# Kernel optimization log

Hardware: AMD Instinct MI355X
Metric: run time of the kernel (lower is better)

Reference implementation:

```python
import jax, jax.numpy as jnp
import numpy as np

D_MODEL = 1024
NUM_HEADS = 16
DEPTH = D_MODEL // NUM_HEADS
B, S = 2, 2048


def setup_inputs() -> dict:
    key = jax.random.key(0)
    ks = jax.random.split(key, 12)
    s = 1.0 / np.sqrt(D_MODEL)
    return {
        "query": jax.random.normal(ks[0], (B, S, D_MODEL), jnp.float32),
        "key": jax.random.normal(ks[1], (B, S, D_MODEL), jnp.float32),
        "value": jax.random.normal(ks[2], (B, S, D_MODEL), jnp.float32),
        "mask": jax.random.randint(ks[3], (B, S), 0, 2, jnp.int32),
        "Wq": jax.random.normal(ks[4], (D_MODEL, D_MODEL), jnp.float32) * s,
        "bq": jnp.zeros((D_MODEL,), jnp.float32),
        "Wk": jax.random.normal(ks[5], (D_MODEL, D_MODEL), jnp.float32) * s,
        "bk": jnp.zeros((D_MODEL,), jnp.float32),
        "Wv": jax.random.normal(ks[6], (D_MODEL, D_MODEL), jnp.float32) * s,
        "bv": jnp.zeros((D_MODEL,), jnp.float32),
        "Wo": jax.random.normal(ks[7], (D_MODEL, D_MODEL), jnp.float32) * s,
        "bo": jnp.zeros((D_MODEL,), jnp.float32),
    }


def _split_heads(x):
    # [B, S, D] -> [B, H, S, depth]
    b, s, _ = x.shape
    return x.reshape(b, s, NUM_HEADS, DEPTH).transpose(0, 2, 1, 3)


def reference(query, key, value, mask, Wq, bq, Wk, bk, Wv, bv, Wo, bo):
    q = _split_heads(query @ Wq.T + bq)
    k = _split_heads(key @ Wk.T + bk)
    v = _split_heads(value @ Wv.T + bv)
    scale = 1.0 / jnp.sqrt(jnp.float32(DEPTH))
    # [B, H, Sq, Sk]
    logits = jnp.einsum("bhqd,bhkd->bhqk", q, k) * scale
    logits = logits + mask.astype(logits.dtype)[:, None, None, :] * (-1e9)
    attn = jax.nn.softmax(logits, axis=-1)
    out = jnp.einsum("bhqk,bhkd->bhqd", attn, v)
    out = out.transpose(0, 2, 1, 3).reshape(query.shape[0], -1, D_MODEL)
    return out @ Wo.T + bo
```

## Files before the change

kernel.cpp:

```cpp
#include <hip/hip_runtime.h>

typedef _Float16 half8 __attribute__((ext_vector_type(8)));
typedef _Float16 half4 __attribute__((ext_vector_type(4)));
typedef __fp16  fp16x2 __attribute__((ext_vector_type(2)));
typedef float floatx4 __attribute__((ext_vector_type(4)));

#define D_MODEL 1024
#define NHEAD   16
#define DH      64
#define BATCH   2
#define SEQ     2048
#define M_TOT   4096

#define SCALE_L2E 0.18033688011112042f
#define MASK_L2E  (-1.4426950408889634e9f)

#define GLD_LDS16(g, l)                                                          \
  __builtin_amdgcn_global_load_lds(                                              \
      (const __attribute__((address_space(1))) void*)(g),                        \
      (__attribute__((address_space(3))) void*)(l), 16, 0, 0)

__device__ inline half4 pk4(floatx4 v) {
  union { fp16x2 h2[2]; half4 h4; } u;
  u.h2[0] = __builtin_amdgcn_cvt_pkrtz(v[0], v[1]);
  u.h2[1] = __builtin_amdgcn_cvt_pkrtz(v[2], v[3]);
  return u.h4;
}

__global__ __launch_bounds__(256) void cvt_all(const float* __restrict__ q,
                                               const float* __restrict__ k,
                                               const float* __restrict__ v,
                                               const float* __restrict__ wq,
                                               const float* __restrict__ wk,
                                               const float* __restrict__ wv,
                                               const float* __restrict__ wo,
                                               _Float16* __restrict__ Xall,
                                               _Float16* __restrict__ Wall) {
  int bid = blockIdx.x;
  const float* src;
  _Float16* dst;
  if (bid < 6144) {
    int tsr = bid >> 11;
    src = (tsr == 0) ? q : (tsr == 1) ? k : v;
    dst = Xall + (size_t)tsr * 4194304;
    bid &= 2047;
  } else {
    int w = (bid - 6144) >> 9;
    src = (w == 0) ? wq : (w == 1) ? wk : (w == 2) ? wv : wo;
    dst = Wall + (size_t)w * 1048576;
    bid = (bid - 6144) & 511;
  }
  int off = bid * 2048 + threadIdx.x * 8;
  float4 a = *(const float4*)(src + off);
  float4 b = *(const float4*)(src + off + 4);
  half8 h;
  h[0] = (_Float16)a.x; h[1] = (_Float16)a.y; h[2] = (_Float16)a.z; h[3] = (_Float16)a.w;
  h[4] = (_Float16)b.x; h[5] = (_Float16)b.y; h[6] = (_Float16)b.z; h[7] = (_Float16)b.w;
  *(half8*)(dst + off) = h;
}

__global__ __launch_bounds__(256) void gemm_qkv(const _Float16* __restrict__ Xall,
                                                const _Float16* __restrict__ Wall,
                                                const float* __restrict__ bq,
                                                const float* __restrict__ bk,
                                                const float* __restrict__ bv,
                                                _Float16* __restrict__ Obase) {
  __shared__ alignas(16) char smem[32768];
  _Float16 (*As)[64]  = (_Float16(*)[64])smem;
  _Float16 (*Bs)[64]  = (_Float16(*)[64])(smem + 16384);
  _Float16 (*Ts)[136] = (_Float16(*)[136])smem;

  const int z = blockIdx.z;
  const _Float16* X = Xall + (size_t)z * 4194304;
  const _Float16* W = Wall + (size_t)z * 1048576;
  const float* bias = (z == 0) ? bq : (z == 1) ? bk : bv;
  _Float16* out = Obase + (size_t)z * 4194304;

  const int t = threadIdx.x, lane = t & 63, wave = t >> 6;
  const int wr = wave >> 1, wc = wave & 1;
  const int m0 = blockIdx.y * 128, n0 = blockIdx.x * 128;
  const int fr = lane & 15, quad = lane >> 4, rg = quad * 4;
  const int fsw = fr & 7;

  floatx4 acc[4][4];
  for (int i = 0; i < 4; i++)
    for (int j = 0; j < 4; j++) acc[i][j] = (floatx4){0.f, 0.f, 0.f, 0.f};

  const int rl = lane >> 3, pc = lane & 7;
  const int gcol = ((pc ^ rl) * 8);
  const _Float16* gA[4];
  const _Float16* gB[4];
  _Float16* lA[4];
  _Float16* lB[4];
  for (int i = 0; i < 4; i++) {
    int row = wave * 32 + i * 8 + rl;
    gA[i] = X + (size_t)(m0 + row) * 1024 + gcol;
    gB[i] = W + (size_t)(n0 + row) * 1024 + gcol;
    lA[i] = &As[wave * 32 + i * 8][0];
    lB[i] = &Bs[wave * 32 + i * 8][0];
  }

  for (int k0 = 0; k0 < 1024; k0 += 64) {
    for (int i = 0; i < 4; i++) GLD_LDS16(gA[i] + k0, lA[i]);
    for (int i = 0; i < 4; i++) GLD_LDS16(gB[i] + k0, lB[i]);
    __syncthreads();

    for (int kk = 0; kk < 2; kk++) {
      const int csw = (((kk << 2) | quad) ^ fsw) * 8;
      half8 af[4], bw[4];
      for (int i = 0; i < 4; i++) {
        af[i] = *(const half8*)&As[wr * 64 + i * 16 + fr][csw];
        bw[i] = *(const half8*)&Bs[wc * 64 + i * 16 + fr][csw];
      }
      for (int i = 0; i < 4; i++)
        for (int j = 0; j < 4; j++)
          acc[i][j] = __builtin_amdgcn_mfma_f32_16x16x32_f16(af[i], bw[j], acc[i][j], 0, 0, 0);
    }
    __syncthreads();
  }

  if (z != 2) {
    for (int i = 0; i < 4; i++)
      for (int j = 0; j < 4; j++) {
        int n = n0 + wc * 64 + j * 16 + fr;
        float bv2 = bias[n];
        int hh = n >> 6, d = n & 63;
        for (int r = 0; r < 4; r++) {
          int m = m0 + wr * 64 + i * 16 + rg + r;
          int bb = m >> 11, s = m & 2047;
          out[(((size_t)(bb * NHEAD + hh)) * SEQ + s) * DH + d] =
              (_Float16)(acc[i][j][r] + bv2);
        }
      }
  } else {
    const int bb = m0 >> 11, s0 = m0 & 2047;
    for (int p = 0; p < 2; p++) {
      __syncthreads();
      if (wc == p) {
        for (int j = 0; j < 4; j++) {
          float bv2 = bias[n0 + p * 64 + j * 16 + fr];
          for (int i = 0; i < 4; i++)
            for (int r = 0; r < 4; r++)
              Ts[j * 16 + fr][wr * 64 + i * 16 + rg + r] =
                  (_Float16)(acc[i][j][r] + bv2);
        }
      }
      __syncthreads();
      int dd = t >> 2, c4 = (t & 3) * 32;
      int hh = (n0 >> 6) + p;
      _Float16* dst = out + (((size_t)(bb * NHEAD + hh)) * DH + dd) * SEQ + s0;
      for (int u = 0; u < 4; u++)
        *(half8*)(dst + c4 + u * 8) = *(const half8*)&Ts[dd][c4 + u * 8];
    }
  }
}

__global__ __launch_bounds__(256) void gemm_wo(const _Float16* __restrict__ ctx,
                                               const _Float16* __restrict__ W,
                                               const float* __restrict__ bias,
                                               float* __restrict__ out) {
  __shared__ alignas(16) _Float16 As[128][64];
  __shared__ alignas(16) _Float16 Bs[64][64];

  const int t = threadIdx.x, lane = t & 63, wave = t >> 6;
  const int m0 = blockIdx.y * 128, n0 = blockIdx.x * 64;
  const int fr = lane & 15, quad = lane >> 4, rg = quad * 4;
  const int fsw = fr & 7;

  floatx4 acc[2][4];
  for (int i = 0; i < 2; i++)
    for (int j = 0; j < 4; j++) acc[i][j] = (floatx4){0.f, 0.f, 0.f, 0.f};

  const int rl = lane >> 3, pc = lane & 7;
  const int gcol = ((pc ^ rl) * 8);
  const _Float16* gA[4];
  const _Float16* gB[2];
  _Float16* lA[4];
  _Float16* lB[2];
  for (int i = 0; i < 4; i++) {
    int row = wave * 32 + i * 8 + rl;
    gA[i] = ctx + (size_t)(m0 + row) * 1024 + gcol;
    lA[i] = &As[wave * 32 + i * 8][0];
  }
  for (int i = 0; i < 2; i++) {
    int row = wave * 16 + i * 8 + rl;
    gB[i] = W + (size_t)(n0 + row) * 1024 + gcol;
    lB[i] = &Bs[wave * 16 + i * 8][0];
  }

  for (int k0 = 0; k0 < 1024; k0 += 64) {
    for (int i = 0; i < 4; i++) GLD_LDS16(gA[i] + k0, lA[i]);
    for (int i = 0; i < 2; i++) GLD_LDS16(gB[i] + k0, lB[i]);
    __syncthreads();

    for (int kk = 0; kk < 2; kk++) {
      const int csw = (((kk << 2) | quad) ^ fsw) * 8;
      half8 af[2], bw[4];
      for (int i = 0; i < 2; i++)
        af[i] = *(const half8*)&As[wave * 32 + i * 16 + fr][csw];
      for (int j = 0; j < 4; j++)
        bw[j] = *(const half8*)&Bs[j * 16 + fr][csw];
      for (int i = 0; i < 2; i++)
        for (int j = 0; j < 4; j++)
          acc[i][j] = __builtin_amdgcn_mfma_f32_16x16x32_f16(af[i], bw[j], acc[i][j], 0, 0, 0);
    }
    __syncthreads();
  }

  for (int i = 0; i < 2; i++)
    for (int j = 0; j < 4; j++) {
      int n = n0 + j * 16 + fr;
      float bv2 = bias[n];
      for (int r = 0; r < 4; r++) {
        int m = m0 + wave * 32 + i * 16 + rg + r;
        out[(size_t)m * D_MODEL + n] = acc[i][j][r] + bv2;
      }
    }
}

__global__ __launch_bounds__(256) void attn_kernel(const _Float16* __restrict__ Qp,
                                                   const _Float16* __restrict__ Kp,
                                                   const _Float16* __restrict__ VT,
                                                   const int* __restrict__ mask,
                                                   _Float16* __restrict__ ctx) {
  __shared__ alignas(16) _Float16 Ks[128][64];
  __shared__ alignas(16) _Float16 Vt[64][128];
  __shared__ float Msf[128];

  const int b = blockIdx.z, h = blockIdx.y, q0 = blockIdx.x * 128;
  const int t = threadIdx.x, lane = t & 63, wave = t >> 6;
  const int fr = lane & 15, quad = lane >> 4, fc = quad * 8;
  const int fsw = fr & 7;

  const _Float16* Kg  = Kp + (size_t)(b * NHEAD + h) * SEQ * DH;
  const _Float16* VTg = VT + (size_t)(b * NHEAD + h) * DH * SEQ;

  half8 qf[2][2];
  {
    const _Float16* Qgw = Qp + ((size_t)(b * NHEAD + h) * SEQ + q0 + wave * 32) * DH;
    for (int mi = 0; mi < 2; mi++)
      for (int kk = 0; kk < 2; kk++)
        qf[mi][kk] = *(const half8*)(Qgw + (mi * 16 + fr) * DH + kk * 32 + fc);
  }

  float lrow[2] = {0.f, 0.f};
  floatx4 oaccT[4][2];
  for (int dj = 0; dj < 4; dj++)
    for (int mi = 0; mi < 2; mi++) oaccT[dj][mi] = (floatx4){0.f, 0.f, 0.f, 0.f};

  const int skr = t >> 1;
  const int skc = (t & 1) * 4;
  const int svr = t >> 2;
  const int svc = (t & 3) * 4;

  for (int kt = 0; kt < SEQ / 128; kt++) {
    const int k0 = kt * 128;
    {
      const half8* gk = (const half8*)(Kg + (k0 + skr) * 64);
      for (int u = 0; u < 4; u++)
        *(half8*)&Ks[skr][((skc + u) ^ (skr & 7)) * 8] = gk[skc + u];
      const half8* gv = (const half8*)(VTg + (size_t)svr * SEQ + k0);
      for (int u = 0; u < 4; u++)
        *(half8*)&Vt[svr][((svc + u) ^ (svr & 7)) * 8] = gv[svc + u];
      if (t < 128) Msf[t] = (float)mask[b * SEQ + k0 + t] * MASK_L2E;
    }
    __syncthreads();

    floatx4 saT[8][2];
#pragma unroll
    for (int t8 = 0; t8 < 8; t8++) {
      saT[t8][0] = (floatx4){0.f, 0.f, 0.f, 0.f};
      saT[t8][1] = (floatx4){0.f, 0.f, 0.f, 0.f};
      half8 kf0 = *(const half8*)&Ks[t8 * 16 + fr][(quad ^ fsw) * 8];
      half8 kf1 = *(const half8*)&Ks[t8 * 16 + fr][((4 | quad) ^ fsw) * 8];
      saT[t8][0] = __builtin_amdgcn_mfma_f32_16x16x32_f16(kf0, qf[0][0], saT[t8][0], 0, 0, 0);
      saT[t8][1] = __builtin_amdgcn_mfma_f32_16x16x32_f16(kf0, qf[1][0], saT[t8][1], 0, 0, 0);
      saT[t8][0] = __builtin_amdgcn_mfma_f32_16x16x32_f16(kf1, qf[0][1], saT[t8][0], 0, 0, 0);
      saT[t8][1] = __builtin_amdgcn_mfma_f32_16x16x32_f16(kf1, qf[1][1], saT[t8][1], 0, 0, 0);
    }

    floatx4 mk[8];
#pragma unroll
    for (int t8 = 0; t8 < 8; t8++)
      mk[t8] = *(const floatx4*)&Msf[t8 * 16 + quad * 4];

#pragma unroll
    for (int mi = 0; mi < 2; mi++) {
      float rs = 0.f;
#pragma unroll
      for (int t8 = 0; t8 < 8; t8++)
        for (int r = 0; r < 4; r++) {
          float p = exp2f(saT[t8][mi][r] * SCALE_L2E + mk[t8][r]);
          saT[t8][mi][r] = p;
          rs += p;
        }
      lrow[mi] += rs;
    }

#pragma unroll
    for (int t8 = 0; t8 < 8; t8++) {
      half4 pb0 = pk4(saT[t8][0]);
      half4 pb1 = pk4(saT[t8][1]);
      const int ch0 = t8 * 2 + (quad >> 1);
      const int voff = ((ch0 ^ fsw) * 8) + (quad & 1) * 4;
#pragma unroll
      for (int dj = 0; dj < 4; dj++) {
        half4 va = *(const half4*)&Vt[dj * 16 + fr][voff];
        oaccT[dj][0] = __builtin_amdgcn_mfma_f32_16x16x16f16(va, pb0, oaccT[dj][0], 0, 0, 0);
        oaccT[dj][1] = __builtin_amdgcn_mfma_f32_16x16x16f16(va, pb1, oaccT[dj][1], 0, 0, 0);
      }
    }
    __syncthreads();
  }

#pragma unroll
  for (int mi = 0; mi < 2; mi++) {
    float l = lrow[mi];
    l += __shfl_xor(l, 16);
    l += __shfl_xor(l, 32);
    float inv = 1.0f / l;
    int qrow = q0 + wave * 32 + mi * 16 + fr;
    _Float16* o = ctx + ((size_t)b * SEQ + qrow) * D_MODEL + h * DH;
#pragma unroll
    for (int dj = 0; dj < 4; dj++) {
      half4 st;
      for (int r = 0; r < 4; r++) st[r] = (_Float16)(oaccT[dj][mi][r] * inv);
      *(half4*)(o + dj * 16 + quad * 4) = st;
    }
  }
}

extern "C" void kernel_launch(void* const* d_in, const int* in_sizes, int n_in,
                              void* d_out, int out_size, void* d_ws, size_t ws_size,
                              hipStream_t stream) {
  const float* query = (const float*)d_in[0];
  const float* key   = (const float*)d_in[1];
  const float* value = (const float*)d_in[2];
  const int*   mask  = (const int*)d_in[3];
  const float* Wq = (const float*)d_in[4];
  const float* bq = (const float*)d_in[5];
  const float* Wk = (const float*)d_in[6];
  const float* bk = (const float*)d_in[7];
  const float* Wv = (const float*)d_in[8];
  const float* bv = (const float*)d_in[9];
  const float* Wo = (const float*)d_in[10];
  const float* bo = (const float*)d_in[11];

  char* ws = (char*)d_ws;
  _Float16* Xall = (_Float16*)(ws);
  _Float16* Wall = (_Float16*)(ws + (size_t)24 * 1024 * 1024);
  _Float16* Qp   = (_Float16*)(ws + (size_t)32 * 1024 * 1024);
  _Float16* ctx  = (_Float16*)(ws + (size_t)56 * 1024 * 1024);

  _Float16* Kp = Qp + (size_t)4194304;
  _Float16* VT = Qp + (size_t)8388608;

  cvt_all<<<8192, 256, 0, stream>>>(query, key, value, Wq, Wk, Wv, Wo, Xall, Wall);

  gemm_qkv<<<dim3(8, 32, 3), 256, 0, stream>>>(Xall, Wall, bq, bk, bv, Qp);

  attn_kernel<<<dim3(SEQ / 128, NHEAD, BATCH), 256, 0, stream>>>(Qp, Kp, VT, mask, ctx);

  gemm_wo<<<dim3(16, 32), 256, 0, stream>>>(ctx, Wall + (size_t)3 * 1048576, bo, (float*)d_out);
}
```

Before: 256.8 us.

## Double-buffer K/V tiles in attention with async global-to-LDS loads

Converts the attention kernel's K, V and mask staging into a two-stage ping-pong buffer. The next tile is prefetched with global_load_lds direct-to-LDS copies, using pre-swizzled source addresses, while the current tile is being computed, and one barrier per iteration is removed. The goal is to hide global memory latency behind the MFMA and exp work. In exchange, LDS use doubles, which may lower occupancy. Correctness now depends on the implicit wait before the barrier covering the async LDS writes.

```diff
diff --git a/kernel.cpp b/kernel.cpp
--- a/kernel.cpp
+++ b/kernel.cpp
@@ -223,9 +223,9 @@
                                                    const _Float16* __restrict__ VT,
                                                    const int* __restrict__ mask,
                                                    _Float16* __restrict__ ctx) {
-  __shared__ alignas(16) _Float16 Ks[128][64];
-  __shared__ alignas(16) _Float16 Vt[64][128];
-  __shared__ float Msf[128];
+  __shared__ alignas(16) _Float16 Ks[2][128][64];
+  __shared__ alignas(16) _Float16 Vt[2][64][128];
+  __shared__ float Msf[2][128];
 
   const int b = blockIdx.z, h = blockIdx.y, q0 = blockIdx.x * 128;
   const int t = threadIdx.x, lane = t & 63, wave = t >> 6;
@@ -234,6 +234,19 @@
 
   const _Float16* Kg  = Kp + (size_t)(b * NHEAD + h) * SEQ * DH;
   const _Float16* VTg = VT + (size_t)(b * NHEAD + h) * DH * SEQ;
+
+  const _Float16* kG[4];
+  const _Float16* vG[4];
+  {
+    const int kr = lane >> 3, kp = lane & 7;
+    const int vr = lane >> 4, vp = lane & 15;
+    for (int i = 0; i < 4; i++) {
+      int krow = wave * 32 + i * 8 + kr;
+      kG[i] = Kg + (size_t)krow * DH + ((kp ^ kr) * 8);
+      int vrow = wave * 16 + i * 4 + vr;
+      vG[i] = VTg + (size_t)vrow * SEQ + ((vp ^ (vrow & 7)) * 8);
+    }
+  }
 
   half8 qf[2][2];
   {
@@ -248,31 +261,31 @@
   for (int dj = 0; dj < 4; dj++)
     for (int mi = 0; mi < 2; mi++) oaccT[dj][mi] = (floatx4){0.f, 0.f, 0.f, 0.f};
 
-  const int skr = t >> 1;
-  const int skc = (t & 1) * 4;
-  const int svr = t >> 2;
-  const int svc = (t & 3) * 4;
-
+  for (int i = 0; i < 4; i++) GLD_LDS16(kG[i], &Ks[0][wave * 32 + i * 8][0]);
+  for (int i = 0; i < 4; i++) GLD_LDS16(vG[i], &Vt[0][wave * 16 + i * 4][0]);
+  if (t < 128) Msf[0][t] = (float)mask[b * SEQ + t] * MASK_L2E;
+  __syncthreads();
+
+  int cur = 0;
   for (int kt = 0; kt < SEQ / 128; kt++) {
-    const int k0 = kt * 128;
-    {
-      const half8* gk = (const half8*)(Kg + (k0 + skr) * 64);
-      for (int u = 0; u < 4; u++)
-        *(half8*)&Ks[skr][((skc + u) ^ (skr & 7)) * 8] = gk[skc + u];
-      const half8* gv = (const half8*)(VTg + (size_t)svr * SEQ + k0);
-      for (int u = 0; u < 4; u++)
-        *(half8*)&Vt[svr][((svc + u) ^ (svr & 7)) * 8] = gv[svc + u];
-      if (t < 128) Msf[t] = (float)mask[b * SEQ + k0 + t] * MASK_L2E;
-    }
-    __syncthreads();
+    const int nxt = cur ^ 1;
+
+    if (kt + 1 < SEQ / 128) {
+      const int k0n = (kt + 1) * 128;
+      for (int i = 0; i < 4; i++)
+        GLD_LDS16(kG[i] + (size_t)k0n * DH, &Ks[nxt][wave * 32 + i * 8][0]);
+      for (int i = 0; i < 4; i++)
+        GLD_LDS16(vG[i] + k0n, &Vt[nxt][wave * 16 + i * 4][0]);
+      if (t < 128) Msf[nxt][t] = (float)mask[b * SEQ + k0n + t] * MASK_L2E;
+    }
 
     floatx4 saT[8][2];
 #pragma unroll
     for (int t8 = 0; t8 < 8; t8++) {
       saT[t8][0] = (floatx4){0.f, 0.f, 0.f, 0.f};
       saT[t8][1] = (floatx4){0.f, 0.f, 0.f, 0.f};
-      half8 kf0 = *(const half8*)&Ks[t8 * 16 + fr][(quad ^ fsw) * 8];
-      half8 kf1 = *(const half8*)&Ks[t8 * 16 + fr][((4 | quad) ^ fsw) * 8];
+      half8 kf0 = *(const half8*)&Ks[cur][t8 * 16 + fr][(quad ^ fsw) * 8];
+      half8 kf1 = *(const half8*)&Ks[cur][t8 * 16 + fr][((4 | quad) ^ fsw) * 8];
       saT[t8][0] = __builtin_amdgcn_mfma_f32_16x16x32_f16(kf0, qf[0][0], saT[t8][0], 0, 0, 0);
       saT[t8][1] = __builtin_amdgcn_mfma_f32_16x16x32_f16(kf0, qf[1][0], saT[t8][1], 0, 0, 0);
       saT[t8][0] = __builtin_amdgcn_mfma_f32_16x16x32_f16(kf1, qf[0][1], saT[t8][0], 0, 0, 0);
@@ -282,7 +295,7 @@
     floatx4 mk[8];
 #pragma unroll
     for (int t8 = 0; t8 < 8; t8++)
-      mk[t8] = *(const floatx4*)&Msf[t8 * 16 + quad * 4];
+      mk[t8] = *(const floatx4*)&Msf[cur][t8 * 16 + quad * 4];
 
 #pragma unroll
     for (int mi = 0; mi < 2; mi++) {
@@ -305,12 +318,14 @@
       const int voff = ((ch0 ^ fsw) * 8) + (quad & 1) * 4;
 #pragma unroll
       for (int dj = 0; dj < 4; dj++) {
-        half4 va = *(const half4*)&Vt[dj * 16 + fr][voff];
+        half4 va = *(const half4*)&Vt[cur][dj * 16 + fr][voff];
         oaccT[dj][0] = __builtin_amdgcn_mfma_f32_16x16x16f16(va, pb0, oaccT[dj][0], 0, 0, 0);
         oaccT[dj][1] = __builtin_amdgcn_mfma_f32_16x16x16f16(va, pb1, oaccT[dj][1], 0, 0, 0);
       }
     }
-    __syncthreads();
+
+    if (kt + 1 < SEQ / 128) __syncthreads();
+    cur = nxt;
   }
 
 #pragma unroll
```

After: 272.8 us. 6.2% more time.

## Double-buffer K tiles with async global-to-LDS loads and register-staged V prefetch

Applied to the files above, without the earlier changes.

Restructures the attention key loop into a software pipeline. K and mask tiles are double-buffered in LDS, with the next K tile loaded asynchronously via global_load_lds, and the next V tile is prefetched into registers and written to LDS after the current tile's compute. The aim is to overlap global memory latency with MFMA and exp work instead of stalling at the top of each iteration. It costs extra LDS and registers and adds a second barrier per iteration. Correctness also depends on the async LDS writes having completed by the barrier.

```diff
diff --git a/kernel.cpp b/kernel.cpp
--- a/kernel.cpp
+++ b/kernel.cpp
@@ -11,6 +11,7 @@
 #define BATCH   2
 #define SEQ     2048
 #define M_TOT   4096
+#define NT      (SEQ / 128)
 
 #define SCALE_L2E 0.18033688011112042f
 #define MASK_L2E  (-1.4426950408889634e9f)
@@ -223,9 +224,11 @@
                                                    const _Float16* __restrict__ VT,
                                                    const int* __restrict__ mask,
                                                    _Float16* __restrict__ ctx) {
-  __shared__ alignas(16) _Float16 Ks[128][64];
+  __shared__ alignas(16) _Float16 Ks0[128][64];
+  __shared__ alignas(16) _Float16 Ks1[128][64];
   __shared__ alignas(16) _Float16 Vt[64][128];
-  __shared__ float Msf[128];
+  __shared__ float Msf0[128];
+  __shared__ float Msf1[128];
 
   const int b = blockIdx.z, h = blockIdx.y, q0 = blockIdx.x * 128;
   const int t = threadIdx.x, lane = t & 63, wave = t >> 6;
@@ -234,6 +237,17 @@
 
   const _Float16* Kg  = Kp + (size_t)(b * NHEAD + h) * SEQ * DH;
   const _Float16* VTg = VT + (size_t)(b * NHEAD + h) * DH * SEQ;
+
+  const _Float16* kG[4];
+  {
+    const int kr = lane >> 3, kp = lane & 7;
+    for (int i = 0; i < 4; i++) {
+      int krow = wave * 32 + i * 8 + kr;
+      kG[i] = Kg + (size_t)krow * DH + ((kp ^ kr) * 8);
+    }
+  }
+  const int svr = t >> 2;
+  const int svc = (t & 3) * 4;
 
   half8 qf[2][2];
   {
@@ -248,70 +262,83 @@
   for (int dj = 0; dj < 4; dj++)
     for (int mi = 0; mi < 2; mi++) oaccT[dj][mi] = (floatx4){0.f, 0.f, 0.f, 0.f};
 
-  const int skr = t >> 1;
-  const int skc = (t & 1) * 4;
-  const int svr = t >> 2;
-  const int svc = (t & 3) * 4;
-
-  for (int kt = 0; kt < SEQ / 128; kt++) {
-    const int k0 = kt * 128;
-    {
-      const half8* gk = (const half8*)(Kg + (k0 + skr) * 64);
-      for (int u = 0; u < 4; u++)
-        *(half8*)&Ks[skr][((skc + u) ^ (skr & 7)) * 8] = gk[skc + u];
-      const half8* gv = (const half8*)(VTg + (size_t)svr * SEQ + k0);
-      for (int u = 0; u < 4; u++)
-        *(half8*)&Vt[svr][((svc + u) ^ (svr & 7)) * 8] = gv[svc + u];
-      if (t < 128) Msf[t] = (float)mask[b * SEQ + k0 + t] * MASK_L2E;
-    }
-    __syncthreads();
-
-    floatx4 saT[8][2];
-#pragma unroll
-    for (int t8 = 0; t8 < 8; t8++) {
-      saT[t8][0] = (floatx4){0.f, 0.f, 0.f, 0.f};
-      saT[t8][1] = (floatx4){0.f, 0.f, 0.f, 0.f};
-      half8 kf0 = *(const half8*)&Ks[t8 * 16 + fr][(quad ^ fsw) * 8];
-      half8 kf1 = *(const half8*)&Ks[t8 * 16 + fr][((4 | quad) ^ fsw) * 8];
-      saT[t8][0] = __builtin_amdgcn_mfma_f32_16x16x32_f16(kf0, qf[0][0], saT[t8][0], 0, 0, 0);
-      saT[t8][1] = __builtin_amdgcn_mfma_f32_16x16x32_f16(kf0, qf[1][0], saT[t8][1], 0, 0, 0);
-      saT[t8][0] = __builtin_amdgcn_mfma_f32_16x16x32_f16(kf1, qf[0][1], saT[t8][0], 0, 0, 0);
-      saT[t8][1] = __builtin_amdgcn_mfma_f32_16x16x32_f16(kf1, qf[1][1], saT[t8][1], 0, 0, 0);
-    }
-
-    floatx4 mk[8];
-#pragma unroll
-    for (int t8 = 0; t8 < 8; t8++)
-      mk[t8] = *(const floatx4*)&Msf[t8 * 16 + quad * 4];
-
-#pragma unroll
-    for (int mi = 0; mi < 2; mi++) {
-      float rs = 0.f;
-#pragma unroll
-      for (int t8 = 0; t8 < 8; t8++)
-        for (int r = 0; r < 4; r++) {
-          float p = exp2f(saT[t8][mi][r] * SCALE_L2E + mk[t8][r]);
-          saT[t8][mi][r] = p;
-          rs += p;
-        }
-      lrow[mi] += rs;
-    }
-
-#pragma unroll
-    for (int t8 = 0; t8 < 8; t8++) {
-      half4 pb0 = pk4(saT[t8][0]);
-      half4 pb1 = pk4(saT[t8][1]);
-      const int ch0 = t8 * 2 + (quad >> 1);
-      const int voff = ((ch0 ^ fsw) * 8) + (quad & 1) * 4;
-#pragma unroll
-      for (int dj = 0; dj < 4; dj++) {
-        half4 va = *(const half4*)&Vt[dj * 16 + fr][voff];
-        oaccT[dj][0] = __builtin_amdgcn_mfma_f32_16x16x16f16(va, pb0, oaccT[dj][0], 0, 0, 0);
-        oaccT[dj][1] = __builtin_amdgcn_mfma_f32_16x16x16f16(va, pb1, oaccT[dj][1], 0, 0, 0);
-      }
-    }
-    __syncthreads();
-  }
+  half8 vbuf[4];
+
+  for (int i = 0; i < 4; i++) GLD_LDS16(kG[i], &Ks0[wave * 32 + i * 8][0]);
+  if (t < 128) Msf0[t] = (float)mask[b * SEQ + t] * MASK_L2E;
+  {
+    const half8* gv = (const half8*)(VTg + (size_t)svr * SEQ);
+    for (int u = 0; u < 4; u++) vbuf[u] = gv[svc + u];
+  }
+  for (int u = 0; u < 4; u++)
+    *(half8*)&Vt[svr][((svc + u) ^ (svr & 7)) * 8] = vbuf[u];
+  __syncthreads();
+
+#define ATTN_STEP(KS_R, MS_R, KS_W, MS_W, kt)                                   \
+  {                                                                             \
+    const bool more = (kt) + 1 < NT;                                            \
+    if (more) {                                                                 \
+      const int k0n = ((kt) + 1) * 128;                                         \
+      for (int i = 0; i < 4; i++)                                               \
+        GLD_LDS16(kG[i] + (size_t)k0n * DH, &KS_W[wave * 32 + i * 8][0]);       \
+      if (t < 128) MS_W[t] = (float)mask[b * SEQ + k0n + t] * MASK_L2E;         \
+      const half8* gv = (const half8*)(VTg + (size_t)svr * SEQ + k0n);          \
+      for (int u = 0; u < 4; u++) vbuf[u] = gv[svc + u];                        \
+    }                                                                           \
+    floatx4 saT[8][2];                                                          \
+    _Pragma("unroll")                                                           \
+    for (int t8 = 0; t8 < 8; t8++) {                                            \
+      saT[t8][0] = (floatx4){0.f, 0.f, 0.f, 0.f};                               \
+      saT[t8][1] = (floatx4){0.f, 0.f, 0.f, 0.f};                               \
+      half8 kf0 = *(const half8*)&KS_R[t8 * 16 + fr][(quad ^ fsw) * 8];         \
+      half8 kf1 = *(const half8*)&KS_R[t8 * 16 + fr][((4 | quad) ^ fsw) * 8];   \
+      saT[t8][0] = __builtin_amdgcn_mfma_f32_16x16x32_f16(kf0, qf[0][0], saT[t8][0], 0, 0, 0); \
+      saT[t8][1] = __builtin_amdgcn_mfma_f32_16x16x32_f16(kf0, qf[1][0], saT[t8][1], 0, 0, 0); \
+      saT[t8][0] = __builtin_amdgcn_mfma_f32_16x16x32_f16(kf1, qf[0][1], saT[t8][0], 0, 0, 0); \
+      saT[t8][1] = __builtin_amdgcn_mfma_f32_16x16x32_f16(kf1, qf[1][1], saT[t8][1], 0, 0, 0); \
+    }                                                                           \
+    floatx4 mk[8];                                                              \
+    _Pragma("unroll")                                                           \
+    for (int t8 = 0; t8 < 8; t8++)                                              \
+      mk[t8] = *(const floatx4*)&MS_R[t8 * 16 + quad * 4];                      \
+    _Pragma("unroll")                                                           \
+    for (int mi = 0; mi < 2; mi++) {                                            \
+      float rs = 0.f;                                                           \
+      _Pragma("unroll")                                                         \
+      for (int t8 = 0; t8 < 8; t8++)                                            \
+        for (int r = 0; r < 4; r++) {                                           \
+          float p = exp2f(saT[t8][mi][r] * SCALE_L2E + mk[t8][r]);              \
+          saT[t8][mi][r] = p;                                                   \
+          rs += p;                                                              \
+        }                                                                       \
+      lrow[mi] += rs;                                                           \
+    }                                                                           \
+    _Pragma("unroll")                                                           \
+    for (int t8 = 0; t8 < 8; t8++) {                                            \
+      half4 pb0 = pk4(saT[t8][0]);                                              \
+      half4 pb1 = pk4(saT[t8][1]);                                              \
+      const int ch0 = t8 * 2 + (quad >> 1);                                     \
+      const int voff = ((ch0 ^ fsw) * 8) + (quad & 1) * 4;                      \
+      _Pragma("unroll")                                                         \
+      for (int dj = 0; dj < 4; dj++) {                                          \
+        half4 va = *(const half4*)&Vt[dj * 16 + fr][voff];                      \
+        oaccT[dj][0] = __builtin_amdgcn_mfma_f32_16x16x16f16(va, pb0, oaccT[dj][0], 0, 0, 0); \
+        oaccT[dj][1] = __builtin_amdgcn_mfma_f32_16x16x16f16(va, pb1, oaccT[dj][1], 0, 0, 0); \
+      }                                                                         \
+    }                                                                           \
+    __syncthreads();                                                            \
+    if (more) {                                                                 \
+      for (int u = 0; u < 4; u++)                                               \
+        *(half8*)&Vt[svr][((svc + u) ^ (svr & 7)) * 8] = vbuf[u];               \
+      __syncthreads();                                                          \
+    }                                                                           \
+  }
+
+  for (int kt = 0; kt < NT; kt += 2) {
+    ATTN_STEP(Ks0, Msf0, Ks1, Msf1, kt);
+    ATTN_STEP(Ks1, Msf1, Ks0, Msf0, kt + 1);
+  }
+#undef ATTN_STEP
 
 #pragma unroll
   for (int mi = 0; mi < 2; mi++) {
```

Result: slower. 276.9 us (+7.8%).

## Load K/V fragments directly from global memory instead of staging through LDS

Applied to the files above, without the earlier changes.

The attention kernel stops staging K and V^T tiles in shared memory. Each wave now reads its MFMA fragments straight from global memory and relies on L1/L2 caching, which removes the per-tile __syncthreads barriers. The mask for the whole sequence is converted into LDS once, up front, and the grid becomes 1D with head-major block ordering so blocks sharing a head's K/V run close together. It also switches to the raw exp2 builtin. The risk is redundant global/L1 traffic, since all four waves load the same K/V fragments, and small 8-byte V loads with long latency and no explicit prefetch.

```diff
diff --git a/kernel.cpp b/kernel.cpp
--- a/kernel.cpp
+++ b/kernel.cpp
@@ -11,6 +11,7 @@
 #define BATCH   2
 #define SEQ     2048
 #define M_TOT   4096
+#define NT      (SEQ / 128)
 
 #define SCALE_L2E 0.18033688011112042f
 #define MASK_L2E  (-1.4426950408889634e9f)
@@ -223,56 +224,59 @@
                                                    const _Float16* __restrict__ VT,
                                                    const int* __restrict__ mask,
                                                    _Float16* __restrict__ ctx) {
-  __shared__ alignas(16) _Float16 Ks[128][64];
-  __shared__ alignas(16) _Float16 Vt[64][128];
-  __shared__ float Msf[128];
-
-  const int b = blockIdx.z, h = blockIdx.y, q0 = blockIdx.x * 128;
+  __shared__ float Msf[SEQ];
+
+  const int bid = blockIdx.x;
+  const int hh = bid & 31;
+  const int qi = bid >> 5;
+  const int b = hh >> 4, h = hh & 15;
+  const int q0 = qi * 128;
+
   const int t = threadIdx.x, lane = t & 63, wave = t >> 6;
   const int fr = lane & 15, quad = lane >> 4, fc = quad * 8;
-  const int fsw = fr & 7;
-
-  const _Float16* Kg  = Kp + (size_t)(b * NHEAD + h) * SEQ * DH;
-  const _Float16* VTg = VT + (size_t)(b * NHEAD + h) * DH * SEQ;
+
+  const _Float16* Kg  = Kp + (size_t)hh * SEQ * DH;
+  const _Float16* VTg = VT + (size_t)hh * DH * SEQ;
+
+  {
+    const int4* ms = (const int4*)(mask + (size_t)b * SEQ);
+    int4 u0 = ms[t * 2], u1 = ms[t * 2 + 1];
+    float* d = &Msf[t * 8];
+    d[0] = (float)u0.x * MASK_L2E; d[1] = (float)u0.y * MASK_L2E;
+    d[2] = (float)u0.z * MASK_L2E; d[3] = (float)u0.w * MASK_L2E;
+    d[4] = (float)u1.x * MASK_L2E; d[5] = (float)u1.y * MASK_L2E;
+    d[6] = (float)u1.z * MASK_L2E; d[7] = (float)u1.w * MASK_L2E;
+  }
 
   half8 qf[2][2];
   {
-    const _Float16* Qgw = Qp + ((size_t)(b * NHEAD + h) * SEQ + q0 + wave * 32) * DH;
+    const _Float16* Qgw = Qp + ((size_t)hh * SEQ + q0 + wave * 32) * DH;
     for (int mi = 0; mi < 2; mi++)
       for (int kk = 0; kk < 2; kk++)
         qf[mi][kk] = *(const half8*)(Qgw + (mi * 16 + fr) * DH + kk * 32 + fc);
   }
+
+  __syncthreads();
 
   float lrow[2] = {0.f, 0.f};
   floatx4 oaccT[4][2];
   for (int dj = 0; dj < 4; dj++)
     for (int mi = 0; mi < 2; mi++) oaccT[dj][mi] = (floatx4){0.f, 0.f, 0.f, 0.f};
 
-  const int skr = t >> 1;
-  const int skc = (t & 1) * 4;
-  const int svr = t >> 2;
-  const int svc = (t & 3) * 4;
-
-  for (int kt = 0; kt < SEQ / 128; kt++) {
+  const _Float16* kL = Kg + (size_t)fr * DH + fc;
+  const _Float16* vL = VTg + (size_t)fr * SEQ + quad * 4;
+
+  for (int kt = 0; kt < NT; kt++) {
     const int k0 = kt * 128;
-    {
-      const half8* gk = (const half8*)(Kg + (k0 + skr) * 64);
-      for (int u = 0; u < 4; u++)
-        *(half8*)&Ks[skr][((skc + u) ^ (skr & 7)) * 8] = gk[skc + u];
-      const half8* gv = (const half8*)(VTg + (size_t)svr * SEQ + k0);
-      for (int u = 0; u < 4; u++)
-        *(half8*)&Vt[svr][((svc + u) ^ (svr & 7)) * 8] = gv[svc + u];
-      if (t < 128) Msf[t] = (float)mask[b * SEQ + k0 + t] * MASK_L2E;
-    }
-    __syncthreads();
+    const _Float16* kT = kL + (size_t)k0 * DH;
 
     floatx4 saT[8][2];
 #pragma unroll
     for (int t8 = 0; t8 < 8; t8++) {
+      half8 kf0 = *(const half8*)(kT + t8 * 16 * DH);
+      half8 kf1 = *(const half8*)(kT + t8 * 16 * DH + 32);
       saT[t8][0] = (floatx4){0.f, 0.f, 0.f, 0.f};
       saT[t8][1] = (floatx4){0.f, 0.f, 0.f, 0.f};
-      half8 kf0 = *(const half8*)&Ks[t8 * 16 + fr][(quad ^ fsw) * 8];
-      half8 kf1 = *(const half8*)&Ks[t8 * 16 + fr][((4 | quad) ^ fsw) * 8];
       saT[t8][0] = __builtin_amdgcn_mfma_f32_16x16x32_f16(kf0, qf[0][0], saT[t8][0], 0, 0, 0);
       saT[t8][1] = __builtin_amdgcn_mfma_f32_16x16x32_f16(kf0, qf[1][0], saT[t8][1], 0, 0, 0);
       saT[t8][0] = __builtin_amdgcn_mfma_f32_16x16x32_f16(kf1, qf[0][1], saT[t8][0], 0, 0, 0);
@@ -282,7 +286,7 @@
     floatx4 mk[8];
 #pragma unroll
     for (int t8 = 0; t8 < 8; t8++)
-      mk[t8] = *(const floatx4*)&Msf[t8 * 16 + quad * 4];
+      mk[t8] = *(const floatx4*)&Msf[k0 + t8 * 16 + quad * 4];
 
 #pragma unroll
     for (int mi = 0; mi < 2; mi++) {
@@ -290,27 +294,25 @@
 #pragma unroll
       for (int t8 = 0; t8 < 8; t8++)
         for (int r = 0; r < 4; r++) {
-          float p = exp2f(saT[t8][mi][r] * SCALE_L2E + mk[t8][r]);
+          float p = __builtin_amdgcn_exp2f(saT[t8][mi][r] * SCALE_L2E + mk[t8][r]);
           saT[t8][mi][r] = p;
           rs += p;
         }
       lrow[mi] += rs;
     }
 
+    const _Float16* vT = vL + k0;
 #pragma unroll
     for (int t8 = 0; t8 < 8; t8++) {
       half4 pb0 = pk4(saT[t8][0]);
       half4 pb1 = pk4(saT[t8][1]);
-      const int ch0 = t8 * 2 + (quad >> 1);
-      const int voff = ((ch0 ^ fsw) * 8) + (quad & 1) * 4;
 #pragma unroll
       for (int dj = 0; dj < 4; dj++) {
-        half4 va = *(const half4*)&Vt[dj * 16 + fr][voff];
+        half4 va = *(const half4*)(vT + (size_t)dj * 16 * SEQ + t8 * 16);
         oaccT[dj][0] = __builtin_amdgcn_mfma_f32_16x16x16f16(va, pb0, oaccT[dj][0], 0, 0, 0);
         oaccT[dj][1] = __builtin_amdgcn_mfma_f32_16x16x16f16(va, pb1, oaccT[dj][1], 0, 0, 0);
       }
     }
-    __syncthreads();
   }
 
 #pragma unroll
@@ -359,7 +361,7 @@
 
   gemm_qkv<<<dim3(8, 32, 3), 256, 0, stream>>>(Xall, Wall, bq, bk, bv, Qp);
 
-  attn_kernel<<<dim3(SEQ / 128, NHEAD, BATCH), 256, 0, stream>>>(Qp, Kp, VT, mask, ctx);
+  attn_kernel<<<dim3(512), 256, 0, stream>>>(Qp, Kp, VT, mask, ctx);
 
   gemm_wo<<<dim3(16, 32), 256, 0, stream>>>(ctx, Wall + (size_t)3 * 1048576, bo, (float*)d_out);
 }
```

New measurement: 348.3 us. +35.6%, slower.
